# Kernel optimization log

Measured on AMD Instinct MI355X. Metric: run time of the kernel, lower is better.

## Reference

```python
import jax, jax.numpy as jnp
import numpy as np

N_NODES = 10000
N_EDGES = 640000
HIDDEN = 128
OUT = 10

def setup_inputs() -> dict:
    key = jax.random.key(0)
    k1, k2, k3, k4 = jax.random.split(key, 4)
    x = jax.random.normal(k1, (N_NODES, HIDDEN), dtype=jnp.float32)
    edge_index = jax.random.randint(k2, (2, N_EDGES), 0, N_NODES, dtype=jnp.int64)
    # ClassifierMLP2 params: Linear(2*hidden -> hidden) -> ReLU -> Linear(hidden -> out)
    W1 = jax.random.normal(k3, (2 * HIDDEN, HIDDEN), dtype=jnp.float32) / np.sqrt(2 * HIDDEN)
    b1 = jnp.zeros((HIDDEN,), dtype=jnp.float32)
    W2 = jax.random.normal(k4, (HIDDEN, OUT), dtype=jnp.float32) / np.sqrt(HIDDEN)
    b2 = jnp.zeros((OUT,), dtype=jnp.float32)
    return {"x": x, "edge_index": edge_index, "W1": W1, "b1": b1, "W2": W2, "b2": b2}

def reference(x, edge_index, W1, b1, W2, b2):
    # mix_node_features(..., node_feat_mixing='cat'): gather src/dst node
    # embeddings per edge and concatenate along feature dim -> [E, 2*H]
    src, dst = edge_index[0], edge_index[1]
    edges_x = jnp.concatenate([x[src], x[dst]], axis=-1)  # [E, 2H]
    # ClassifierMLP2 (dropout inactive at inference)
    h = jax.nn.relu(edges_x @ W1 + b1)                    # [E, H]
    return h @ W2 + b2                                    # [E, OUT]
```

## Files before the change

kernel.cpp:

```cpp
#include <hip/hip_runtime.h>


typedef _Float16 f16;
typedef _Float16 f16x8 __attribute__((ext_vector_type(8)));
typedef float    f32x4 __attribute__((ext_vector_type(4)));

#define HID  128
#define TWOH 256
#define OUTD 10

__global__ __launch_bounds__(256) void node_AB(
    const float* __restrict__ x,
    const float* __restrict__ W1,
    const float* __restrict__ b1,
    f16* __restrict__ AB,
    int n_nodes)
{
    const int t = threadIdx.x;
    const int lane = t & 63;
    const int r = lane & 15, g = lane >> 4;
    const int wv = t >> 6;
    const int n0 = blockIdx.x * 16;
    const int c0 = wv * 64;

    f16x8 w1f[4][4];
#pragma unroll
    for (int ct = 0; ct < 4; ++ct) {
        const int c = c0 + ct * 16 + r;
        const float* wp = (c < HID) ? (W1 + c) : (W1 + HID * HID + (c - HID));
#pragma unroll
        for (int st = 0; st < 4; ++st) {
            f16x8 v;
#pragma unroll
            for (int j = 0; j < 8; ++j)
                v[j] = (f16)wp[(long)(st * 32 + g * 8 + j) * HID];
            w1f[ct][st] = v;
        }
    }

    const int xrow = (n0 + r < n_nodes) ? (n0 + r) : (n_nodes - 1);
    f32x4 acc[4] = {{0,0,0,0},{0,0,0,0},{0,0,0,0},{0,0,0,0}};
#pragma unroll
    for (int st = 0; st < 4; ++st) {
        const float* xp = x + (long)xrow * HID + st * 32 + g * 8;
        const float4 x0 = *(const float4*)xp;
        const float4 x1 = *(const float4*)(xp + 4);
        f16x8 a;
        a[0] = (f16)x0.x; a[1] = (f16)x0.y; a[2] = (f16)x0.z; a[3] = (f16)x0.w;
        a[4] = (f16)x1.x; a[5] = (f16)x1.y; a[6] = (f16)x1.z; a[7] = (f16)x1.w;
#pragma unroll
        for (int ct = 0; ct < 4; ++ct)
            acc[ct] = __builtin_amdgcn_mfma_f32_16x16x32_f16(a, w1f[ct][st], acc[ct], 0, 0, 0);
    }

#pragma unroll
    for (int ct = 0; ct < 4; ++ct) {
        const int c = c0 + ct * 16 + r;
        const float bias = (c < HID) ? b1[c] : 0.f;
#pragma unroll
        for (int q = 0; q < 4; ++q) {
            const int node = n0 + g * 4 + q;
            if (node < n_nodes)
                AB[(long)node * TWOH + c] = (f16)(acc[ct][q] + bias);
        }
    }
}

__global__ __launch_bounds__(256) void edge_mlp(
    const f16* __restrict__ AB,
    const int* __restrict__ ei,
    const float* __restrict__ W2,
    const float* __restrict__ b2,
    float* __restrict__ out,
    int n_edges)
{
    const int t = threadIdx.x;
    const int lane = t & 63;
    const int r = lane & 15, g = lane >> 4;
    const int wv = t >> 6;

    const bool cok = (r < OUTD);
    const int cw = cok ? r : 0;
    f16x8 w2f[4];
#pragma unroll
    for (int st = 0; st < 4; ++st) {
        f16x8 v;
#pragma unroll
        for (int j = 0; j < 8; ++j) {
            const float w = W2[(long)(st * 32 + g * 8 + j) * OUTD + cw];
            v[j] = cok ? (f16)w : (f16)0.f;
        }
        w2f[st] = v;
    }
    const float bj = cok ? b2[r] : 0.f;

    const f16x8* __restrict__ ABv = (const f16x8*)AB;
    const long eb = (long)blockIdx.x * 256 + wv * 64;

#pragma unroll
    for (int it = 0; it < 4; ++it) {
        const long e = eb + it * 16 + r;
        const long ec = (e < n_edges) ? e : (n_edges - 1);
        const int sn = ei[ec];
        const int dn = ei[(long)n_edges + ec];

        f32x4 acc = {0, 0, 0, 0};
#pragma unroll
        for (int st = 0; st < 4; ++st) {
            const f16x8 a = ABv[(long)sn * 32 + st * 4 + g];
            const f16x8 c = ABv[(long)dn * 32 + 16 + st * 4 + g];
            f16x8 s = a + c;
            const f16x8 z = {0, 0, 0, 0, 0, 0, 0, 0};
            s = __builtin_elementwise_max(s, z);
            acc = __builtin_amdgcn_mfma_f32_16x16x32_f16(s, w2f[st], acc, 0, 0, 0);
        }

        if (cok) {
            const long er = eb + it * 16 + g * 4;
#pragma unroll
            for (int q = 0; q < 4; ++q) {
                const long ee = er + q;
                if (ee < n_edges)
                    out[ee * OUTD + r] = acc[q] + bj;
            }
        }
    }
}

extern "C" void kernel_launch(void* const* d_in, const int* in_sizes, int n_in,
                              void* d_out, int out_size, void* d_ws, size_t ws_size,
                              hipStream_t stream) {
    const float* x  = (const float*)d_in[0];
    const int*   ei = (const int*)d_in[1];
    const float* W1 = (const float*)d_in[2];
    const float* b1 = (const float*)d_in[3];
    const float* W2 = (const float*)d_in[4];
    const float* b2 = (const float*)d_in[5];
    float* out = (float*)d_out;

    const int n_nodes = in_sizes[0] / HID;
    const int n_edges = in_sizes[1] / 2;

    f16* AB = (f16*)d_ws;

    node_AB<<<(n_nodes + 15) / 16, 256, 0, stream>>>(x, W1, b1, AB, n_nodes);

    edge_mlp<<<(n_edges + 255) / 256, 256, 0, stream>>>(AB, ei, W2, b2, out, n_edges);
}
```

Measured before the change: 70.60 us.

## Pre-transpose W1, persist node tiles, prefetch gathers and stage coalesced output stores

Adds a small kernel that transposes W1 to f16 once, so node_AB loads its weight fragments as vectors instead of strided scalar reads. node_AB now loops over two tiles per block, spreading the weight load across more work. edge_mlp handles 512 edges per block with all indices loaded up front, double-buffers the AB gathers for the next edge group, and writes outputs through shared memory as coalesced float4 stores. The cost is an extra kernel launch, higher register pressure, and fewer blocks in both kernels.

```diff
diff --git a/kernel.cpp b/kernel.cpp
--- a/kernel.cpp
+++ b/kernel.cpp
@@ -9,59 +9,68 @@
 #define TWOH 256
 #define OUTD 10
 
+__global__ __launch_bounds__(256) void w1_transpose(
+    const float* __restrict__ W1,
+    f16* __restrict__ W1T)
+{
+    const int idx = blockIdx.x * 256 + threadIdx.x;
+    const int c = idx >> 7, k = idx & 127;
+    const float v = (c < HID) ? W1[k * HID + c]
+                              : W1[(HID + k) * HID + (c - HID)];
+    W1T[idx] = (f16)v;
+}
+
 __global__ __launch_bounds__(256) void node_AB(
     const float* __restrict__ x,
-    const float* __restrict__ W1,
+    const f16* __restrict__ W1T,
     const float* __restrict__ b1,
     f16* __restrict__ AB,
-    int n_nodes)
+    int n_nodes, int n_tiles)
 {
     const int t = threadIdx.x;
     const int lane = t & 63;
     const int r = lane & 15, g = lane >> 4;
     const int wv = t >> 6;
-    const int n0 = blockIdx.x * 16;
     const int c0 = wv * 64;
 
     f16x8 w1f[4][4];
+    float bias[4];
 #pragma unroll
     for (int ct = 0; ct < 4; ++ct) {
         const int c = c0 + ct * 16 + r;
-        const float* wp = (c < HID) ? (W1 + c) : (W1 + HID * HID + (c - HID));
+        bias[ct] = (c < HID) ? b1[c] : 0.f;
+#pragma unroll
+        for (int st = 0; st < 4; ++st)
+            w1f[ct][st] = *(const f16x8*)(W1T + (long)c * HID + st * 32 + g * 8);
+    }
+
+    for (int tile = blockIdx.x; tile < n_tiles; tile += gridDim.x) {
+        const int n0 = tile * 16;
+        const int xrow = (n0 + r < n_nodes) ? (n0 + r) : (n_nodes - 1);
+
+        f32x4 acc[4] = {{0,0,0,0},{0,0,0,0},{0,0,0,0},{0,0,0,0}};
 #pragma unroll
         for (int st = 0; st < 4; ++st) {
-            f16x8 v;
+            const float* xp = x + (long)xrow * HID + st * 32 + g * 8;
+            const float4 x0 = *(const float4*)xp;
+            const float4 x1 = *(const float4*)(xp + 4);
+            f16x8 a;
+            a[0] = (f16)x0.x; a[1] = (f16)x0.y; a[2] = (f16)x0.z; a[3] = (f16)x0.w;
+            a[4] = (f16)x1.x; a[5] = (f16)x1.y; a[6] = (f16)x1.z; a[7] = (f16)x1.w;
 #pragma unroll
-            for (int j = 0; j < 8; ++j)
-                v[j] = (f16)wp[(long)(st * 32 + g * 8 + j) * HID];
-            w1f[ct][st] = v;
+            for (int ct = 0; ct < 4; ++ct)
+                acc[ct] = __builtin_amdgcn_mfma_f32_16x16x32_f16(a, w1f[ct][st], acc[ct], 0, 0, 0);
         }
-    }
-
-    const int xrow = (n0 + r < n_nodes) ? (n0 + r) : (n_nodes - 1);
-    f32x4 acc[4] = {{0,0,0,0},{0,0,0,0},{0,0,0,0},{0,0,0,0}};
-#pragma unroll
-    for (int st = 0; st < 4; ++st) {
-        const float* xp = x + (long)xrow * HID + st * 32 + g * 8;
-        const float4 x0 = *(const float4*)xp;
-        const float4 x1 = *(const float4*)(xp + 4);
-        f16x8 a;
-        a[0] = (f16)x0.x; a[1] = (f16)x0.y; a[2] = (f16)x0.z; a[3] = (f16)x0.w;
-        a[4] = (f16)x1.x; a[5] = (f16)x1.y; a[6] = (f16)x1.z; a[7] = (f16)x1.w;
-#pragma unroll
-        for (int ct = 0; ct < 4; ++ct)
-            acc[ct] = __builtin_amdgcn_mfma_f32_16x16x32_f16(a, w1f[ct][st], acc[ct], 0, 0, 0);
-    }
 
 #pragma unroll
-    for (int ct = 0; ct < 4; ++ct) {
-        const int c = c0 + ct * 16 + r;
-        const float bias = (c < HID) ? b1[c] : 0.f;
+        for (int ct = 0; ct < 4; ++ct) {
+            const int c = c0 + ct * 16 + r;
 #pragma unroll
-        for (int q = 0; q < 4; ++q) {
-            const int node = n0 + g * 4 + q;
-            if (node < n_nodes)
-                AB[(long)node * TWOH + c] = (f16)(acc[ct][q] + bias);
+            for (int q = 0; q < 4; ++q) {
+                const int node = n0 + g * 4 + q;
+                if (node < n_nodes)
+                    AB[(long)node * TWOH + c] = (f16)(acc[ct][q] + bias[ct]);
+            }
         }
     }
 }
@@ -74,6 +83,7 @@
     float* __restrict__ out,
     int n_edges)
 {
+    __shared__ float stage[4][160];
     const int t = threadIdx.x;
     const int lane = t & 63;
     const int r = lane & 15, g = lane >> 4;
@@ -95,33 +105,62 @@
     const float bj = cok ? b2[r] : 0.f;
 
     const f16x8* __restrict__ ABv = (const f16x8*)AB;
-    const long eb = (long)blockIdx.x * 256 + wv * 64;
+    const long eb = (long)blockIdx.x * 512 + wv * 128;
+
+    int sn[8], dn[8];
+#pragma unroll
+    for (int it = 0; it < 8; ++it) {
+        const long e = eb + it * 16 + r;
+        const long ec = (e < n_edges) ? e : (n_edges - 1);
+        sn[it] = ei[ec];
+        dn[it] = ei[(long)n_edges + ec];
+    }
+
+    f16x8 pa[2][4], pc[2][4];
+#pragma unroll
+    for (int st = 0; st < 4; ++st) {
+        pa[0][st] = ABv[(long)sn[0] * 32 + st * 4 + g];
+        pc[0][st] = ABv[(long)dn[0] * 32 + 16 + st * 4 + g];
+    }
 
 #pragma unroll
-    for (int it = 0; it < 4; ++it) {
-        const long e = eb + it * 16 + r;
-        const long ec = (e < n_edges) ? e : (n_edges - 1);
-        const int sn = ei[ec];
-        const int dn = ei[(long)n_edges + ec];
+    for (int it = 0; it < 8; ++it) {
+        const int cur = it & 1, nxt = cur ^ 1;
+        if (it < 7) {
+            const long an = (long)sn[it + 1] * 32, bn = (long)dn[it + 1] * 32;
+#pragma unroll
+            for (int st = 0; st < 4; ++st) {
+                pa[nxt][st] = ABv[an + st * 4 + g];
+                pc[nxt][st] = ABv[bn + 16 + st * 4 + g];
+            }
+        }
 
+        const f16x8 z = {0, 0, 0, 0, 0, 0, 0, 0};
         f32x4 acc = {0, 0, 0, 0};
 #pragma unroll
         for (int st = 0; st < 4; ++st) {
-            const f16x8 a = ABv[(long)sn * 32 + st * 4 + g];
-            const f16x8 c = ABv[(long)dn * 32 + 16 + st * 4 + g];
-            f16x8 s = a + c;
-            const f16x8 z = {0, 0, 0, 0, 0, 0, 0, 0};
-            s = __builtin_elementwise_max(s, z);
+            const f16x8 s = __builtin_elementwise_max(pa[cur][st] + pc[cur][st], z);
             acc = __builtin_amdgcn_mfma_f32_16x16x32_f16(s, w2f[st], acc, 0, 0, 0);
         }
 
-        if (cok) {
-            const long er = eb + it * 16 + g * 4;
+        const long base = eb + (long)it * 16;
+        if (base + 16 <= n_edges) {
+            if (cok) {
+#pragma unroll
+                for (int q = 0; q < 4; ++q)
+                    stage[wv][(g * 4 + q) * OUTD + r] = acc[q] + bj;
+            }
+            __builtin_amdgcn_wave_barrier();
+            if (lane < 40) {
+                const float4 vv = *(const float4*)&stage[wv][lane * 4];
+                *(float4*)(out + base * OUTD + lane * 4) = vv;
+            }
+            __builtin_amdgcn_wave_barrier();
+        } else if (cok) {
 #pragma unroll
             for (int q = 0; q < 4; ++q) {
-                const long ee = er + q;
-                if (ee < n_edges)
-                    out[ee * OUTD + r] = acc[q] + bj;
+                const long ee = base + g * 4 + q;
+                if (ee < n_edges) out[ee * OUTD + r] = acc[q] + bj;
             }
         }
     }
@@ -140,10 +179,15 @@
 
     const int n_nodes = in_sizes[0] / HID;
     const int n_edges = in_sizes[1] / 2;
+    const int n_tiles = (n_nodes + 15) / 16;
 
-    f16* AB = (f16*)d_ws;
+    f16* AB  = (f16*)d_ws;
+    f16* W1T = AB + (long)n_nodes * TWOH;
 
-    node_AB<<<(n_nodes + 15) / 16, 256, 0, stream>>>(x, W1, b1, AB, n_nodes);
+    w1_transpose<<<(TWOH * HID) / 256, 256, 0, stream>>>(W1, W1T);
 
-    edge_mlp<<<(n_edges + 255) / 256, 256, 0, stream>>>(AB, ei, W2, b2, out, n_edges);
+    int nb = (n_tiles + 1) / 2;
+    node_AB<<<nb, 256, 0, stream>>>(x, W1T, b1, AB, n_nodes, n_tiles);
+
+    edge_mlp<<<(n_edges + 511) / 512, 256, 0, stream>>>(AB, ei, W2, b2, out, n_edges);
 }
```

Result: faster. 66.58 us (-5.7%).
